# Performance work log

Hardware: AMD Instinct MI355X
Metric: run time of the kernel (lower is better)

Reference implementation:

```python
import jax, jax.numpy as jnp
import numpy as np


def setup_inputs() -> dict:
    key = jax.random.key(0)
    k_x, k1, k2, k3 = jax.random.split(key, 4)
    dim, hidden, out_dim = 4096, 8192, 4096
    x = jax.random.normal(k_x, (4, 2048, dim), dtype=jnp.float32)
    # VNNILinear initializes weight = randn(out, in) * 0.02
    w1 = jax.random.normal(k1, (hidden, dim), dtype=jnp.float32) * 0.02
    w2 = jax.random.normal(k2, (out_dim, hidden), dtype=jnp.float32) * 0.02
    w3 = jax.random.normal(k3, (hidden, dim), dtype=jnp.float32) * 0.02
    return {"x": x, "w1": w1, "w2": w2, "w3": w3}


def _quant_linear(x, w):
    """Emulate VNNILinear int8 weight-quantized matmul (inference path).

    Per-output-channel symmetric quant: scale = max|w_row| / 127,
    w_q = round(w / scale) in int8, y = x @ (w_q * scale).T.
    """
    w_max = jnp.clip(jnp.max(jnp.abs(w), axis=1, keepdims=True), 1e-6)  # [out,1]
    scale_w = w_max / 127.0
    w_q = jnp.round(w / scale_w).astype(jnp.int8)
    w_dq = w_q.astype(jnp.float32) * scale_w  # dequantized weight
    return jnp.einsum('bsd,hd->bsh', x, w_dq)


def reference(x, w1, w2, w3):
    # SwiGLU: w2( silu(w1(x)) * w3(x) ), all bias-free, int8 VNNI weight quant
    h = jax.nn.silu(_quant_linear(x, w1)) * _quant_linear(x, w3)  # [B,S,hidden]
    return _quant_linear(h, w2)  # [B,S,out_dim]
```

## Files before the change

kernel.cpp:

```cpp
#include <hip/hip_runtime.h>
#include <hip/hip_bf16.h>
#include <stdint.h>


typedef short bf16x8 __attribute__((ext_vector_type(8)));
typedef float f32x4  __attribute__((ext_vector_type(4)));
typedef float f32x16 __attribute__((ext_vector_type(16)));
typedef int   i32x4  __attribute__((ext_vector_type(4)));
typedef int   i32x16 __attribute__((ext_vector_type(16)));

__device__ __forceinline__ unsigned short f2bf(float f) {
  unsigned u = __builtin_bit_cast(unsigned, f);
  u += 0x7FFFu + ((u >> 16) & 1u);
  return (unsigned short)(u >> 16);
}

#define GLOAD_LDS16(gaddr, laddr)                                             \
  __builtin_amdgcn_global_load_lds(                                           \
      (const __attribute__((address_space(1))) void*)(gaddr),                 \
      (__attribute__((address_space(3))) void*)(laddr), 16, 0, 0)

#define FENCE()      asm volatile("" ::: "memory")
#define BAR()        __builtin_amdgcn_s_barrier()
#define WAIT_LGKM0() asm volatile("s_waitcnt lgkmcnt(0)" ::: "memory")
#define WAIT_VM8()   asm volatile("s_waitcnt vmcnt(8)" ::: "memory")
#define WAIT_VM4()   asm volatile("s_waitcnt vmcnt(4)" ::: "memory")
#define WAIT_VM2()   asm volatile("s_waitcnt vmcnt(2)" ::: "memory")
#define WAIT_VM0()   asm volatile("s_waitcnt vmcnt(0)" ::: "memory")
#define SFENCE()     __builtin_amdgcn_sched_barrier(0)


__global__ void quant_rows_i8_kernel(const float* __restrict__ w,
                                     char* __restrict__ q,
                                     float* __restrict__ scale, int cols,
                                     float clip) {
  const int row = blockIdx.x;
  const float* wr = w + (size_t)row * cols;
  char* qr = q + (size_t)row * cols;

  float m = 0.f;
  for (int c = threadIdx.x * 4; c < cols; c += blockDim.x * 4) {
    float4 v = *reinterpret_cast<const float4*>(wr + c);
    m = fmaxf(m, fmaxf(fmaxf(fabsf(v.x), fabsf(v.y)),
                       fmaxf(fabsf(v.z), fabsf(v.w))));
  }
#pragma unroll
  for (int off = 32; off; off >>= 1) m = fmaxf(m, __shfl_xor(m, off));
  __shared__ float smax[4];
  if ((threadIdx.x & 63) == 0) smax[threadIdx.x >> 6] = m;
  __syncthreads();
  m = fmaxf(fmaxf(smax[0], smax[1]), fmaxf(smax[2], smax[3]));

  const float s = fmaxf(m, clip) / 127.0f;
  if (threadIdx.x == 0) scale[row] = s;
  for (int c = threadIdx.x * 4; c < cols; c += blockDim.x * 4) {
    float4 v = *reinterpret_cast<const float4*>(wr + c);
    int b0 = (int)rintf(v.x / s), b1 = (int)rintf(v.y / s);
    int b2 = (int)rintf(v.z / s), b3 = (int)rintf(v.w / s);
    unsigned pk = (b0 & 0xff) | ((b1 & 0xff) << 8) | ((b2 & 0xff) << 16)
                  | ((b3 & 0xff) << 24);
    *reinterpret_cast<unsigned*>(qr + c) = pk;
  }
}

__global__ void quant_rows_bf16_kernel(const float* __restrict__ w,
                                       unsigned short* __restrict__ wq,
                                       int cols) {
  const int row = blockIdx.x;
  const float* wr = w + (size_t)row * cols;
  unsigned short* wqr = wq + (size_t)row * cols;

  float m = 0.f;
  for (int c = threadIdx.x * 4; c < cols; c += blockDim.x * 4) {
    float4 v = *reinterpret_cast<const float4*>(wr + c);
    m = fmaxf(m, fmaxf(fmaxf(fabsf(v.x), fabsf(v.y)),
                       fmaxf(fabsf(v.z), fabsf(v.w))));
  }
#pragma unroll
  for (int off = 32; off; off >>= 1) m = fmaxf(m, __shfl_xor(m, off));
  __shared__ float smax[4];
  if ((threadIdx.x & 63) == 0) smax[threadIdx.x >> 6] = m;
  __syncthreads();
  m = fmaxf(fmaxf(smax[0], smax[1]), fmaxf(smax[2], smax[3]));

  const float s = fmaxf(m, 1e-6f) / 127.0f;
  for (int c = threadIdx.x * 4; c < cols; c += blockDim.x * 4) {
    float4 v = *reinterpret_cast<const float4*>(wr + c);
    ushort4 o;
    o.x = f2bf(rintf(v.x / s) * s);
    o.y = f2bf(rintf(v.y / s) * s);
    o.z = f2bf(rintf(v.z / s) * s);
    o.w = f2bf(rintf(v.w / s) * s);
    *reinterpret_cast<ushort4*>(wqr + c) = o;
  }
}


__device__ __forceinline__ void xcd_swizzle(int& bx, int& by, int gx, int gy) {
  int nwg = gx * gy;
  int bid = by * gx + bx;
  int cpx = nwg >> 3;
  int s = (bid & 7) * cpx + (bid >> 3);
  by = s / gx;
  bx = s % gx;
}

__global__ __launch_bounds__(512, 2)
void gemm_i8_swiglu_kernel(const char* __restrict__ Aq,
                           const char* __restrict__ B1q,
                           const char* __restrict__ B3q,
                           const float* __restrict__ sx,
                           const float* __restrict__ sw1,
                           const float* __restrict__ sw3,
                           unsigned short* __restrict__ H,
                           int M, int N, int K) {
  __shared__ alignas(1024) char lds[65536];

  int bx = blockIdx.x, by = blockIdx.y;
  xcd_swizzle(bx, by, gridDim.x, gridDim.y);
  const int brow = by * 256, bcol = bx * 128;

  const int t = threadIdx.x, lane = t & 63, w = t >> 6;
  const int wr = w >> 2, wc = w & 3;
  const int l31 = lane & 31, hi = lane >> 5;
  const int NT = K >> 5;

  const int gc16 = (((t & 1) ^ ((t >> 3) & 1))) * 16;
  const char* srcA = Aq + (size_t)(brow + (t >> 1)) * K + gc16;
  const char* srcB = (t < 256 ? B1q : B3q)
                   + (size_t)(bcol + ((t & 255) >> 1)) * K + gc16;

#define STAGE(kt)                                                             \
  {                                                                           \
    const int s2 = ((kt) & 3) * 16384;                                        \
    const size_t ko = (size_t)(kt) * 32;                                      \
    GLOAD_LDS16(srcA + ko, lds + s2 + t * 16);                                \
    GLOAD_LDS16(srcB + ko, lds + s2 + 8192 + t * 16);                         \
  }

  STAGE(0); STAGE(1); STAGE(2);
  WAIT_VM4();
  FENCE(); BAR();

  i32x16 acc[4][2] = {};
  const int aoff = (wr * 128 + l31) * 32 + ((hi ^ ((l31 >> 2) & 1)) * 16);
  const int boff1 = 8192 + (wc * 32 + l31) * 32
                    + ((hi ^ ((l31 >> 2) & 1)) * 16);
  const int boff3 = boff1 + 4096;

  for (int k = 0; k < NT; ++k) {
    const char* sl = lds + (k & 3) * 16384;
    i32x4 afr[4], b1f, b3f;
#pragma unroll
    for (int m = 0; m < 4; ++m)
      afr[m] = *reinterpret_cast<const i32x4*>(sl + aoff + m * 1024);
    b1f = *reinterpret_cast<const i32x4*>(sl + boff1);
    b3f = *reinterpret_cast<const i32x4*>(sl + boff3);
    if (k + 3 < NT) {
      STAGE(k + 3);
      WAIT_VM4();
    } else if (k == NT - 3) {
      WAIT_VM2();
    } else {
      WAIT_VM0();
    }
    FENCE(); BAR();
    WAIT_LGKM0(); SFENCE();
    __builtin_amdgcn_s_setprio(1);
#pragma unroll
    for (int m = 0; m < 4; ++m) {
      acc[m][0] = __builtin_amdgcn_mfma_i32_32x32x32_i8(afr[m], b1f,
                                                        acc[m][0], 0, 0, 0);
      acc[m][1] = __builtin_amdgcn_mfma_i32_32x32x32_i8(afr[m], b3f,
                                                        acc[m][1], 0, 0, 0);
    }
    __builtin_amdgcn_s_setprio(0);
    FENCE(); BAR();
  }
#undef STAGE

  const int ocol = bcol + wc * 32 + l31;
  const int rowb = brow + wr * 128 + 4 * hi;
  const float sw1c = sw1[ocol], sw3c = sw3[ocol];
#pragma unroll
  for (int m = 0; m < 4; ++m) {
#pragma unroll
    for (int rq = 0; rq < 4; ++rq) {
      const int r0 = rowb + m * 32 + 8 * rq;
      const f32x4 sx4 = *reinterpret_cast<const f32x4*>(sx + r0);
#pragma unroll
      for (int j = 0; j < 4; ++j) {
        float y1 = (float)acc[m][0][rq * 4 + j] * (sx4[j] * sw1c);
        float y3 = (float)acc[m][1][rq * 4 + j] * (sx4[j] * sw3c);
        float hv = (y1 / (1.f + __expf(-y1))) * y3;
        H[(size_t)(r0 + j) * N + ocol] = f2bf(hv);
      }
    }
  }
}

__global__ __launch_bounds__(512, 2)
void gemm_bf16_kernel(const unsigned short* __restrict__ A,
                      const unsigned short* __restrict__ B,
                      float* __restrict__ C, int M, int N, int K) {
  __shared__ alignas(1024) unsigned short lds[65536];

  int bx = blockIdx.x, by = blockIdx.y;
  xcd_swizzle(bx, by, gridDim.x, gridDim.y);
  const int brow = by * 256, bcol = bx * 256;

  const int t = threadIdx.x, lane = t & 63, w = t >> 6;
  const int wr = w >> 2, wc = w & 3;
  const int l31 = lane & 31, hi = lane >> 5, rx3 = lane & 3;
  const int NT = K >> 5;

  const int rS = t >> 2;
  const int cS = ((t & 3) ^ ((t >> 2) & 3)) * 8;
  const unsigned short* srcA = A + (size_t)(brow + rS) * K + cS;
  const unsigned short* srcB = B + (size_t)(bcol + rS) * K + cS;

#define STAGE_A(kt)                                                           \
  {                                                                           \
    const int s2 = ((kt) & 3) * 16384;                                        \
    const size_t ko = (size_t)(kt) * 32;                                      \
    GLOAD_LDS16(srcA + ko, &lds[s2 + t * 8]);                                 \
    GLOAD_LDS16(srcA + (size_t)128 * K + ko, &lds[s2 + 4096 + t * 8]);        \
  }
#define STAGE_B(kt)                                                           \
  {                                                                           \
    const int s2 = ((kt) & 3) * 16384;                                        \
    const size_t ko = (size_t)(kt) * 32;                                      \
    GLOAD_LDS16(srcB + ko, &lds[s2 + 8192 + t * 8]);                          \
    GLOAD_LDS16(srcB + (size_t)128 * K + ko, &lds[s2 + 12288 + t * 8]);       \
  }

  STAGE_A(0); STAGE_B(0);
  STAGE_A(1); STAGE_B(1);
  STAGE_A(2); STAGE_B(2);
  WAIT_VM8();
  FENCE(); BAR();

  f32x16 acc[4][2] = {};
  int aIdx[4][2], bIdx[2][2];
#pragma unroll
  for (int m = 0; m < 4; ++m)
#pragma unroll
    for (int kh = 0; kh < 2; ++kh)
      aIdx[m][kh] = (wr * 128 + l31 + m * 32) * 32
                    + (((2 * kh + hi) ^ rx3) * 8);
#pragma unroll
  for (int n = 0; n < 2; ++n)
#pragma unroll
    for (int kh = 0; kh < 2; ++kh)
      bIdx[n][kh] = 8192 + (wc * 64 + l31 + n * 32) * 32
                    + (((2 * kh + hi) ^ rx3) * 8);

  for (int k = 0; k < NT; ++k) {
    const unsigned short* sl = &lds[(k & 3) * 16384];
    const bool pf = (k + 3 < NT);
    bf16x8 afr[2][2], bfr[2][2];

#pragma unroll
    for (int m = 0; m < 2; ++m)
#pragma unroll
      for (int kh = 0; kh < 2; ++kh)
        afr[m][kh] = *reinterpret_cast<const bf16x8*>(sl + aIdx[m][kh]);
#pragma unroll
    for (int n = 0; n < 2; ++n)
#pragma unroll
      for (int kh = 0; kh < 2; ++kh)
        bfr[n][kh] = *reinterpret_cast<const bf16x8*>(sl + bIdx[n][kh]);
    if (pf) STAGE_A(k + 3);
    FENCE(); BAR();
    WAIT_LGKM0(); SFENCE();
    __builtin_amdgcn_s_setprio(1);
#pragma unroll
    for (int m = 0; m < 2; ++m)
#pragma unroll
      for (int n = 0; n < 2; ++n)
#pragma unroll
        for (int kh = 0; kh < 2; ++kh)
          acc[m][n] = __builtin_amdgcn_mfma_f32_32x32x16_bf16(
              afr[m][kh], bfr[n][kh], acc[m][n], 0, 0, 0);
    __builtin_amdgcn_s_setprio(0);
    FENCE(); BAR();

#pragma unroll
    for (int m = 0; m < 2; ++m)
#pragma unroll
      for (int kh = 0; kh < 2; ++kh)
        afr[m][kh] = *reinterpret_cast<const bf16x8*>(sl + aIdx[m + 2][kh]);
    if (pf) {
      STAGE_B(k + 3);
      WAIT_VM8();
    } else if (k == NT - 3) {
      WAIT_VM4();
    } else {
      WAIT_VM0();
    }
    FENCE(); BAR();
    WAIT_LGKM0(); SFENCE();
    __builtin_amdgcn_s_setprio(1);
#pragma unroll
    for (int m = 0; m < 2; ++m)
#pragma unroll
      for (int n = 0; n < 2; ++n)
#pragma unroll
        for (int kh = 0; kh < 2; ++kh)
          acc[m + 2][n] = __builtin_amdgcn_mfma_f32_32x32x16_bf16(
              afr[m][kh], bfr[n][kh], acc[m + 2][n], 0, 0, 0);
    __builtin_amdgcn_s_setprio(0);
    FENCE(); BAR();
  }
#undef STAGE_A
#undef STAGE_B

  const int ocol = bcol + wc * 64 + l31;
  const int rowb = brow + wr * 128 + 4 * hi;
#pragma unroll
  for (int m = 0; m < 4; ++m)
#pragma unroll
    for (int n = 0; n < 2; ++n)
#pragma unroll
      for (int rq = 0; rq < 4; ++rq)
#pragma unroll
        for (int j = 0; j < 4; ++j)
          C[(size_t)(rowb + m * 32 + 8 * rq + j) * N + (ocol + n * 32)] =
              acc[m][n][rq * 4 + j];
}


extern "C" void kernel_launch(void* const* d_in, const int* in_sizes, int n_in,
                              void* d_out, int out_size, void* d_ws,
                              size_t ws_size, hipStream_t stream) {
  const float* x  = (const float*)d_in[0];
  const float* w1 = (const float*)d_in[1];
  const float* w2 = (const float*)d_in[2];
  const float* w3 = (const float*)d_in[3];
  float* out = (float*)d_out;

  const int DIM = 4096, HID = 8192;
  const int M = in_sizes[0] / DIM;

  char* xq  = (char*)d_ws;
  char* w1q = xq + (size_t)M * DIM;
  char* w3q = w1q + (size_t)HID * DIM;
  unsigned short* w2b = (unsigned short*)(w3q + (size_t)HID * DIM);
  unsigned short* h = w2b + (size_t)DIM * HID;
  float* sx  = (float*)(h + (size_t)M * HID);
  float* sw1 = sx + M;
  float* sw3 = sw1 + HID;

  quant_rows_i8_kernel<<<HID, 256, 0, stream>>>(w1, w1q, sw1, DIM, 1e-6f);
  quant_rows_i8_kernel<<<HID, 256, 0, stream>>>(w3, w3q, sw3, DIM, 1e-6f);
  quant_rows_i8_kernel<<<M, 256, 0, stream>>>(x, xq, sx, DIM, 1e-30f);
  quant_rows_bf16_kernel<<<DIM, 256, 0, stream>>>(w2, w2b, HID);

  gemm_i8_swiglu_kernel<<<dim3(HID / 128, M / 256), 512, 0, stream>>>(
      xq, w1q, w3q, sx, sw1, sw3, h, M, HID, DIM);
  gemm_bf16_kernel<<<dim3(DIM / 256, M / 256), 512, 0, stream>>>(
      h, w2b, out, M, DIM, HID);
}
```

Baseline: 1.513 ms.

## Double-buffer MFMA fragments in registers and halve barriers in both GEMMs

```diff
diff --git a/kernel.cpp b/kernel.cpp
--- a/kernel.cpp
+++ b/kernel.cpp
@@ -23,9 +23,9 @@
 #define FENCE()      asm volatile("" ::: "memory")
 #define BAR()        __builtin_amdgcn_s_barrier()
 #define WAIT_LGKM0() asm volatile("s_waitcnt lgkmcnt(0)" ::: "memory")
+#define WAIT_LGKM6() asm volatile("s_waitcnt lgkmcnt(6)" ::: "memory")
 #define WAIT_VM8()   asm volatile("s_waitcnt vmcnt(8)" ::: "memory")
 #define WAIT_VM4()   asm volatile("s_waitcnt vmcnt(4)" ::: "memory")
-#define WAIT_VM2()   asm volatile("s_waitcnt vmcnt(2)" ::: "memory")
 #define WAIT_VM0()   asm volatile("s_waitcnt vmcnt(0)" ::: "memory")
 #define SFENCE()     __builtin_amdgcn_sched_barrier(0)
 
@@ -114,7 +114,7 @@
                            const float* __restrict__ sw3,
                            unsigned short* __restrict__ H,
                            int M, int N, int K) {
-  __shared__ alignas(1024) char lds[65536];
+  __shared__ alignas(1024) char lds[131072];
 
   int bx = blockIdx.x, by = blockIdx.y;
   xcd_swizzle(bx, by, gridDim.x, gridDim.y);
@@ -123,115 +123,27 @@
   const int t = threadIdx.x, lane = t & 63, w = t >> 6;
   const int wr = w >> 2, wc = w & 3;
   const int l31 = lane & 31, hi = lane >> 5;
-  const int NT = K >> 5;
-
-  const int gc16 = (((t & 1) ^ ((t >> 3) & 1))) * 16;
-  const char* srcA = Aq + (size_t)(brow + (t >> 1)) * K + gc16;
-  const char* srcB = (t < 256 ? B1q : B3q)
-                   + (size_t)(bcol + ((t & 255) >> 1)) * K + gc16;
-
-#define STAGE(kt)                                                             \
-  {                                                                           \
-    const int s2 = ((kt) & 3) * 16384;                                        \
-    const size_t ko = (size_t)(kt) * 32;                                      \
-    GLOAD_LDS16(srcA + ko, lds + s2 + t * 16);                                \
-    GLOAD_LDS16(srcB + ko, lds + s2 + 8192 + t * 16);                         \
-  }
-
-  STAGE(0); STAGE(1); STAGE(2);
-  WAIT_VM4();
-  FENCE(); BAR();
-
-  i32x16 acc[4][2] = {};
-  const int aoff = (wr * 128 + l31) * 32 + ((hi ^ ((l31 >> 2) & 1)) * 16);
-  const int boff1 = 8192 + (wc * 32 + l31) * 32
-                    + ((hi ^ ((l31 >> 2) & 1)) * 16);
-  const int boff3 = boff1 + 4096;
-
-  for (int k = 0; k < NT; ++k) {
-    const char* sl = lds + (k & 3) * 16384;
-    i32x4 afr[4], b1f, b3f;
-#pragma unroll
-    for (int m = 0; m < 4; ++m)
-      afr[m] = *reinterpret_cast<const i32x4*>(sl + aoff + m * 1024);
-    b1f = *reinterpret_cast<const i32x4*>(sl + boff1);
-    b3f = *reinterpret_cast<const i32x4*>(sl + boff3);
-    if (k + 3 < NT) {
-      STAGE(k + 3);
-      WAIT_VM4();
-    } else if (k == NT - 3) {
-      WAIT_VM2();
-    } else {
-      WAIT_VM0();
-    }
-    FENCE(); BAR();
-    WAIT_LGKM0(); SFENCE();
-    __builtin_amdgcn_s_setprio(1);
-#pragma unroll
-    for (int m = 0; m < 4; ++m) {
-      acc[m][0] = __builtin_amdgcn_mfma_i32_32x32x32_i8(afr[m], b1f,
-                                                        acc[m][0], 0, 0, 0);
-      acc[m][1] = __builtin_amdgcn_mfma_i32_32x32x32_i8(afr[m], b3f,
-                                                        acc[m][1], 0, 0, 0);
-    }
-    __builtin_amdgcn_s_setprio(0);
-    FENCE(); BAR();
-  }
-#undef STAGE
-
-  const int ocol = bcol + wc * 32 + l31;
-  const int rowb = brow + wr * 128 + 4 * hi;
-  const float sw1c = sw1[ocol], sw3c = sw3[ocol];
-#pragma unroll
-  for (int m = 0; m < 4; ++m) {
-#pragma unroll
-    for (int rq = 0; rq < 4; ++rq) {
-      const int r0 = rowb + m * 32 + 8 * rq;
-      const f32x4 sx4 = *reinterpret_cast<const f32x4*>(sx + r0);
-#pragma unroll
-      for (int j = 0; j < 4; ++j) {
-        float y1 = (float)acc[m][0][rq * 4 + j] * (sx4[j] * sw1c);
-        float y3 = (float)acc[m][1][rq * 4 + j] * (sx4[j] * sw3c);
-        float hv = (y1 / (1.f + __expf(-y1))) * y3;
-        H[(size_t)(r0 + j) * N + ocol] = f2bf(hv);
-      }
-    }
-  }
-}
-
-__global__ __launch_bounds__(512, 2)
-void gemm_bf16_kernel(const unsigned short* __restrict__ A,
-                      const unsigned short* __restrict__ B,
-                      float* __restrict__ C, int M, int N, int K) {
-  __shared__ alignas(1024) unsigned short lds[65536];
-
-  int bx = blockIdx.x, by = blockIdx.y;
-  xcd_swizzle(bx, by, gridDim.x, gridDim.y);
-  const int brow = by * 256, bcol = bx * 256;
-
-  const int t = threadIdx.x, lane = t & 63, w = t >> 6;
-  const int wr = w >> 2, wc = w & 3;
-  const int l31 = lane & 31, hi = lane >> 5, rx3 = lane & 3;
-  const int NT = K >> 5;
+  const int NT = K >> 6;
 
   const int rS = t >> 2;
-  const int cS = ((t & 3) ^ ((t >> 2) & 3)) * 8;
-  const unsigned short* srcA = A + (size_t)(brow + rS) * K + cS;
-  const unsigned short* srcB = B + (size_t)(bcol + rS) * K + cS;
+  const int gcS = ((t & 3) ^ (rS & 3)) * 16;
+  const char* srcA  = Aq  + (size_t)(brow + rS) * K + gcS;
+  const char* srcB1 = B1q + (size_t)(bcol + rS) * K + gcS;
+  const char* srcB3 = B3q + (size_t)(bcol + rS) * K + gcS;
 
 #define STAGE_A(kt)                                                           \
   {                                                                           \
-    const int s2 = ((kt) & 3) * 16384;                                        \
-    const size_t ko = (size_t)(kt) * 32;                                      \
-    GLOAD_LDS16(srcA + ko, &lds[s2 + t * 8]);                                 \
-    GLOAD_LDS16(srcA + (size_t)128 * K + ko, &lds[s2 + 4096 + t * 8]);        \
+    const int s2 = ((kt) & 3) * 32768;                                        \
+    const size_t ko = (size_t)(kt) * 64;                                      \
+    GLOAD_LDS16(srcA + ko, lds + s2 + t * 16);                                \
+    GLOAD_LDS16(srcA + (size_t)128 * K + ko, lds + s2 + 8192 + t * 16);       \
   }
 #define STAGE_B(kt)                                                           \
   {                                                                           \
-    const int s2 = ((kt) & 3) * 16384;                                        \
-    const size_t ko = (size_t)(kt) * 32;                                      \
-    GLOAD_LDS16(srcB + ko, &lds[s2 + 8192 + t * 8]);                          \
-    GLOAD_LDS16(srcB + (size_t)128 * K + ko, &lds[s2 + 12288 + t * 8]);       \
+    const int s2 = ((kt) & 3) * 32768;                                        \
+    const size_t ko = (size_t)(kt) * 64;                                      \
+    GLOAD_LDS16(srcB1 + ko, lds + s2 + 16384 + t * 16);                       \
+    GLOAD_LDS16(srcB3 + ko, lds + s2 + 24576 + t * 16);                       \
   }
 
   STAGE_A(0); STAGE_B(0);
@@ -240,56 +152,43 @@
   WAIT_VM8();
   FENCE(); BAR();
 
-  f32x16 acc[4][2] = {};
-  int aIdx[4][2], bIdx[2][2];
+  const int cx = l31 & 3;
+  const int aoff  = (wr * 128 + l31) * 64 + ((hi ^ cx) * 16);
+  const int boff1 = 16384 + (wc * 32 + l31) * 64 + ((hi ^ cx) * 16);
+  const int boff3 = boff1 + 8192;
+
+  i32x16 acc[4][2] = {};
+  i32x4 a0[4], b10, b30;
+  i32x4 a1[4], b11, b31;
+
 #pragma unroll
   for (int m = 0; m < 4; ++m)
-#pragma unroll
-    for (int kh = 0; kh < 2; ++kh)
-      aIdx[m][kh] = (wr * 128 + l31 + m * 32) * 32
-                    + (((2 * kh + hi) ^ rx3) * 8);
-#pragma unroll
-  for (int n = 0; n < 2; ++n)
-#pragma unroll
-    for (int kh = 0; kh < 2; ++kh)
-      bIdx[n][kh] = 8192 + (wc * 64 + l31 + n * 32) * 32
-                    + (((2 * kh + hi) ^ rx3) * 8);
+    a0[m] = *reinterpret_cast<const i32x4*>(lds + aoff + m * 2048);
+  b10 = *reinterpret_cast<const i32x4*>(lds + boff1);
+  b30 = *reinterpret_cast<const i32x4*>(lds + boff3);
 
   for (int k = 0; k < NT; ++k) {
-    const unsigned short* sl = &lds[(k & 3) * 16384];
+    const char* sl = lds + (k & 3) * 32768;
     const bool pf = (k + 3 < NT);
-    bf16x8 afr[2][2], bfr[2][2];
-
-#pragma unroll
-    for (int m = 0; m < 2; ++m)
-#pragma unroll
-      for (int kh = 0; kh < 2; ++kh)
-        afr[m][kh] = *reinterpret_cast<const bf16x8*>(sl + aIdx[m][kh]);
-#pragma unroll
-    for (int n = 0; n < 2; ++n)
-#pragma unroll
-      for (int kh = 0; kh < 2; ++kh)
-        bfr[n][kh] = *reinterpret_cast<const bf16x8*>(sl + bIdx[n][kh]);
+
+#pragma unroll
+    for (int m = 0; m < 4; ++m)
+      a1[m] = *reinterpret_cast<const i32x4*>(sl + (aoff ^ 32) + m * 2048);
+    b11 = *reinterpret_cast<const i32x4*>(sl + (boff1 ^ 32));
+    b31 = *reinterpret_cast<const i32x4*>(sl + (boff3 ^ 32));
     if (pf) STAGE_A(k + 3);
-    FENCE(); BAR();
-    WAIT_LGKM0(); SFENCE();
+    WAIT_LGKM6();
+    SFENCE();
     __builtin_amdgcn_s_setprio(1);
 #pragma unroll
-    for (int m = 0; m < 2; ++m)
-#pragma unroll
-      for (int n = 0; n < 2; ++n)
-#pragma unroll
-        for (int kh = 0; kh < 2; ++kh)
-          acc[m][n] = __builtin_amdgcn_mfma_f32_32x32x16_bf16(
-              afr[m][kh], bfr[n][kh], acc[m][n], 0, 0, 0);
+    for (int m = 0; m < 4; ++m) {
+      acc[m][0] = __builtin_amdgcn_mfma_i32_32x32x32_i8(a0[m], b10,
+                                                        acc[m][0], 0, 0, 0);
+      acc[m][1] = __builtin_amdgcn_mfma_i32_32x32x32_i8(a0[m], b30,
+                                                        acc[m][1], 0, 0, 0);
+    }
     __builtin_amdgcn_s_setprio(0);
-    FENCE(); BAR();
-
-#pragma unroll
-    for (int m = 0; m < 2; ++m)
-#pragma unroll
-      for (int kh = 0; kh < 2; ++kh)
-        afr[m][kh] = *reinterpret_cast<const bf16x8*>(sl + aIdx[m + 2][kh]);
+
     if (pf) {
       STAGE_B(k + 3);
       WAIT_VM8();
@@ -298,19 +197,155 @@
     } else {
       WAIT_VM0();
     }
+    WAIT_LGKM0();
     FENCE(); BAR();
-    WAIT_LGKM0(); SFENCE();
+    if (k + 1 < NT) {
+      const char* sn = lds + ((k + 1) & 3) * 32768;
+#pragma unroll
+      for (int m = 0; m < 4; ++m)
+        a0[m] = *reinterpret_cast<const i32x4*>(sn + aoff + m * 2048);
+      b10 = *reinterpret_cast<const i32x4*>(sn + boff1);
+      b30 = *reinterpret_cast<const i32x4*>(sn + boff3);
+    }
+    SFENCE();
     __builtin_amdgcn_s_setprio(1);
 #pragma unroll
-    for (int m = 0; m < 2; ++m)
-#pragma unroll
-      for (int n = 0; n < 2; ++n)
-#pragma unroll
-        for (int kh = 0; kh < 2; ++kh)
-          acc[m + 2][n] = __builtin_amdgcn_mfma_f32_32x32x16_bf16(
-              afr[m][kh], bfr[n][kh], acc[m + 2][n], 0, 0, 0);
+    for (int m = 0; m < 4; ++m) {
+      acc[m][0] = __builtin_amdgcn_mfma_i32_32x32x32_i8(a1[m], b11,
+                                                        acc[m][0], 0, 0, 0);
+      acc[m][1] = __builtin_amdgcn_mfma_i32_32x32x32_i8(a1[m], b31,
+                                                        acc[m][1], 0, 0, 0);
+    }
     __builtin_amdgcn_s_setprio(0);
+  }
+#undef STAGE_A
+#undef STAGE_B
+
+  const int ocol = bcol + wc * 32 + l31;
+  const int rowb = brow + wr * 128 + 4 * hi;
+  const float sw1c = sw1[ocol], sw3c = sw3[ocol];
+#pragma unroll
+  for (int m = 0; m < 4; ++m) {
+#pragma unroll
+    for (int rq = 0; rq < 4; ++rq) {
+      const int r0 = rowb + m * 32 + 8 * rq;
+      const f32x4 sx4 = *reinterpret_cast<const f32x4*>(sx + r0);
+#pragma unroll
+      for (int j = 0; j < 4; ++j) {
+        float y1 = (float)acc[m][0][rq * 4 + j] * (sx4[j] * sw1c);
+        float y3 = (float)acc[m][1][rq * 4 + j] * (sx4[j] * sw3c);
+        float hv = (y1 / (1.f + __expf(-y1))) * y3;
+        H[(size_t)(r0 + j) * N + ocol] = f2bf(hv);
+      }
+    }
+  }
+}
+
+__global__ __launch_bounds__(512, 2)
+void gemm_bf16_kernel(const unsigned short* __restrict__ A,
+                      const unsigned short* __restrict__ B,
+                      float* __restrict__ C, int M, int N, int K) {
+  __shared__ alignas(1024) unsigned short lds[65536];
+
+  int bx = blockIdx.x, by = blockIdx.y;
+  xcd_swizzle(bx, by, gridDim.x, gridDim.y);
+  const int brow = by * 256, bcol = bx * 256;
+
+  const int t = threadIdx.x, lane = t & 63, w = t >> 6;
+  const int wr = w >> 2, wc = w & 3;
+  const int l31 = lane & 31, hi = lane >> 5;
+  const int NT = K >> 5;
+
+  const int rS = t >> 2;
+  const int cS = ((t & 3) ^ (rS & 3)) * 8;
+  const unsigned short* srcA = A + (size_t)(brow + rS) * K + cS;
+  const unsigned short* srcB = B + (size_t)(bcol + rS) * K + cS;
+
+#define STAGE_A(kt)                                                           \
+  {                                                                           \
+    const int s2 = ((kt) & 3) * 16384;                                        \
+    const size_t ko = (size_t)(kt) * 32;                                      \
+    GLOAD_LDS16(srcA + ko, &lds[s2 + t * 8]);                                 \
+    GLOAD_LDS16(srcA + (size_t)128 * K + ko, &lds[s2 + 4096 + t * 8]);        \
+  }
+#define STAGE_B(kt)                                                           \
+  {                                                                           \
+    const int s2 = ((kt) & 3) * 16384;                                        \
+    const size_t ko = (size_t)(kt) * 32;                                      \
+    GLOAD_LDS16(srcB + ko, &lds[s2 + 8192 + t * 8]);                          \
+    GLOAD_LDS16(srcB + (size_t)128 * K + ko, &lds[s2 + 12288 + t * 8]);       \
+  }
+
+  STAGE_A(0); STAGE_B(0);
+  STAGE_A(1); STAGE_B(1);
+  STAGE_A(2); STAGE_B(2);
+  WAIT_VM8();
+  FENCE(); BAR();
+
+  const int cx = l31 & 3;
+  const int aoff  = (wr * 128 + l31) * 32 + ((hi ^ cx) * 8);
+  const int boff0 = 8192 + (wc * 64 + l31) * 32 + ((hi ^ cx) * 8);
+
+  f32x16 acc[4][2] = {};
+  bf16x8 a0[4], b00, b01;
+  bf16x8 a1[4], b10, b11;
+
+#pragma unroll
+  for (int m = 0; m < 4; ++m)
+    a0[m] = *reinterpret_cast<const bf16x8*>(&lds[aoff + m * 1024]);
+  b00 = *reinterpret_cast<const bf16x8*>(&lds[boff0]);
+  b01 = *reinterpret_cast<const bf16x8*>(&lds[boff0 + 1024]);
+
+  for (int k = 0; k < NT; ++k) {
+    const unsigned short* sl = &lds[(k & 3) * 16384];
+    const bool pf = (k + 3 < NT);
+
+#pragma unroll
+    for (int m = 0; m < 4; ++m)
+      a1[m] = *reinterpret_cast<const bf16x8*>(sl + (aoff ^ 16) + m * 1024);
+    b10 = *reinterpret_cast<const bf16x8*>(sl + (boff0 ^ 16));
+    b11 = *reinterpret_cast<const bf16x8*>(sl + ((boff0 + 1024) ^ 16));
+    if (pf) STAGE_A(k + 3);
+    WAIT_LGKM6();
+    SFENCE();
+    __builtin_amdgcn_s_setprio(1);
+#pragma unroll
+    for (int m = 0; m < 4; ++m) {
+      acc[m][0] = __builtin_amdgcn_mfma_f32_32x32x16_bf16(a0[m], b00,
+                                                          acc[m][0], 0, 0, 0);
+      acc[m][1] = __builtin_amdgcn_mfma_f32_32x32x16_bf16(a0[m], b01,
+                                                          acc[m][1], 0, 0, 0);
+    }
+    __builtin_amdgcn_s_setprio(0);
+
+    if (pf) {
+      STAGE_B(k + 3);
+      WAIT_VM8();
+    } else if (k == NT - 3) {
+      WAIT_VM4();
+    } else {
+      WAIT_VM0();
+    }
+    WAIT_LGKM0();
     FENCE(); BAR();
+    if (k + 1 < NT) {
+      const unsigned short* sn = &lds[((k + 1) & 3) * 16384];
+#pragma unroll
+      for (int m = 0; m < 4; ++m)
+        a0[m] = *reinterpret_cast<const bf16x8*>(sn + aoff + m * 1024);
+      b00 = *reinterpret_cast<const bf16x8*>(sn + boff0);
+      b01 = *reinterpret_cast<const bf16x8*>(sn + boff0 + 1024);
+    }
+    SFENCE();
+    __builtin_amdgcn_s_setprio(1);
+#pragma unroll
+    for (int m = 0; m < 4; ++m) {
+      acc[m][0] = __builtin_amdgcn_mfma_f32_32x32x16_bf16(a1[m], b10,
+                                                          acc[m][0], 0, 0, 0);
+      acc[m][1] = __builtin_amdgcn_mfma_f32_32x32x16_bf16(a1[m], b11,
+                                                          acc[m][1], 0, 0, 0);
+    }
+    __builtin_amdgcn_s_setprio(0);
   }
 #undef STAGE_A
 #undef STAGE_B
```

Result: faster. 1.396 ms (-7.7%).
